# Performance work log

Hardware: AMD Instinct MI355X
Metric: run time of the kernel (lower is better)

The kernel has to match this reference:

```python
import jax, jax.numpy as jnp
import numpy as np

N_NODES = 100000
N_EDGES = 2000000
D_IN = 4
HID = 64


def setup_inputs() -> dict:
    key = jax.random.key(0)
    ks = jax.random.split(key, 8)
    node_feats = jax.random.normal(ks[0], (N_NODES, D_IN), dtype=jnp.float32)
    pairs = jax.random.randint(ks[1], (N_EDGES, 2), 0, N_NODES, dtype=jnp.int64)
    # Kaiming-ish init scaling
    W1 = jax.random.normal(ks[2], (D_IN, HID), dtype=jnp.float32) / np.sqrt(D_IN)
    b1 = jnp.zeros((HID,), dtype=jnp.float32)
    W2 = jax.random.normal(ks[3], (HID, HID), dtype=jnp.float32) / np.sqrt(HID)
    b2 = jnp.zeros((HID,), dtype=jnp.float32)
    We1 = jax.random.normal(ks[4], (3 * HID, HID), dtype=jnp.float32) / np.sqrt(3 * HID)
    be1 = jnp.zeros((HID,), dtype=jnp.float32)
    We2 = jax.random.normal(ks[5], (HID, 1), dtype=jnp.float32) / np.sqrt(HID)
    be2 = jnp.zeros((1,), dtype=jnp.float32)
    return {"node_feats": node_feats, "pairs": pairs, "W1": W1, "b1": b1,
            "W2": W2, "b2": b2, "We1": We1, "be1": be1, "We2": We2, "be2": be2}


def reference(node_feats, pairs, W1, b1, W2, b2, We1, be1, We2, be2):
    # node MLP: Linear -> ReLU -> Linear -> ReLU
    H = jax.nn.relu(node_feats @ W1 + b1)      # [N, HID]
    H = jax.nn.relu(H @ W2 + b2)               # [N, HID]
    # vectorized gather over all edge pairs (replaces Python loop)
    hu = H[pairs[:, 0]]                        # [E, HID]
    hv = H[pairs[:, 1]]                        # [E, HID]
    E = jnp.concatenate([hu, hv, jnp.abs(hu - hv)], axis=-1)  # [E, 3*HID]
    # edge MLP: Linear -> ReLU -> Linear, squeeze last dim
    scores = (jax.nn.relu(E @ We1 + be1) @ We2 + be2)[:, 0]   # [E]
    return scores
```

## Files before the change

### kernel.cpp

```cpp
#include <hip/hip_runtime.h>

#define N_NODES 100000
#define N_EDGES 2000000

typedef __bf16 bf16x8 __attribute__((ext_vector_type(8)));
typedef float f32x4 __attribute__((ext_vector_type(4)));
typedef float f32x16 __attribute__((ext_vector_type(16)));
typedef unsigned short u16x2 __attribute__((ext_vector_type(2)));

#define AS1 __attribute__((address_space(1)))
#define AS3 __attribute__((address_space(3)))

__device__ __forceinline__ unsigned f2bf_rne(float f) {
  unsigned u = __builtin_bit_cast(unsigned, f);
  u += 0x7FFFu + ((u >> 16) & 1u);
  return u >> 16;
}

__device__ __forceinline__ unsigned pack_rhu(float lo, float hi) {
  unsigned ulo = __builtin_bit_cast(unsigned, lo) + 0x8000u;
  unsigned uhi = __builtin_bit_cast(unsigned, hi) + 0x8000u;
  return __builtin_amdgcn_perm(uhi, ulo, 0x07060302u);
}

__device__ __forceinline__ unsigned pk_max_u16(unsigned a, unsigned b) {
  u16x2 r = __builtin_elementwise_max(__builtin_bit_cast(u16x2, a),
                                      __builtin_bit_cast(u16x2, b));
  return __builtin_bit_cast(unsigned, r);
}
__device__ __forceinline__ unsigned pk_min_u16(unsigned a, unsigned b) {
  u16x2 r = __builtin_elementwise_min(__builtin_bit_cast(u16x2, a),
                                      __builtin_bit_cast(u16x2, b));
  return __builtin_bit_cast(unsigned, r);
}

__global__ __launch_bounds__(64, 1) void node_mfma_kernel(
    const float* __restrict__ X, const float* __restrict__ W1,
    const float* __restrict__ b1, const float* __restrict__ W2,
    const float* __restrict__ b2, unsigned short* __restrict__ H) {
  const int lane = threadIdx.x;
  const int l15 = lane & 15;
  const int quad = lane >> 4;

  float w1v[2][4][8], b1v[2][8];
#pragma unroll
  for (int c = 0; c < 2; ++c)
#pragma unroll
    for (int j = 0; j < 8; ++j) {
      int col = c * 32 + quad * 8 + j;
      b1v[c][j] = b1[col];
#pragma unroll
      for (int d = 0; d < 4; ++d) w1v[c][d][j] = W1[d * 64 + col];
    }

  uint4 afr[2][4];
#pragma unroll
  for (int c = 0; c < 2; ++c)
#pragma unroll
    for (int mt = 0; mt < 4; ++mt) {
      unsigned w[4];
#pragma unroll
      for (int p = 0; p < 4; ++p) {
        int k = c * 32 + quad * 8 + 2 * p;
        unsigned lo = f2bf_rne(W2[k * 64 + mt * 16 + l15]);
        unsigned hi = f2bf_rne(W2[(k + 1) * 64 + mt * 16 + l15]);
        w[p] = lo | (hi << 16);
      }
      afr[c][mt] = make_uint4(w[0], w[1], w[2], w[3]);
    }
  float b2v[16];
#pragma unroll
  for (int mt = 0; mt < 4; ++mt)
#pragma unroll
    for (int r = 0; r < 4; ++r) b2v[mt * 4 + r] = b2[mt * 16 + quad * 4 + r];

  const int ntiles = N_NODES / 16;
  for (int tile = blockIdx.x; tile < ntiles; tile += gridDim.x) {
    float4 xv = ((const float4*)X)[tile * 16 + l15];

    uint4 bfr[2];
#pragma unroll
    for (int c = 0; c < 2; ++c) {
      unsigned w[4];
#pragma unroll
      for (int p = 0; p < 4; ++p) {
        float h0 = fmaxf(b1v[c][2 * p] + xv.x * w1v[c][0][2 * p] +
                             xv.y * w1v[c][1][2 * p] + xv.z * w1v[c][2][2 * p] +
                             xv.w * w1v[c][3][2 * p],
                         0.f);
        float h1 = fmaxf(b1v[c][2 * p + 1] + xv.x * w1v[c][0][2 * p + 1] +
                             xv.y * w1v[c][1][2 * p + 1] +
                             xv.z * w1v[c][2][2 * p + 1] +
                             xv.w * w1v[c][3][2 * p + 1],
                         0.f);
        w[p] = pack_rhu(h0, h1);
      }
      bfr[c] = make_uint4(w[0], w[1], w[2], w[3]);
    }

    f32x4 acc[4];
#pragma unroll
    for (int mt = 0; mt < 4; ++mt) acc[mt] = (f32x4){0.f, 0.f, 0.f, 0.f};
#pragma unroll
    for (int c = 0; c < 2; ++c)
#pragma unroll
      for (int mt = 0; mt < 4; ++mt)
        acc[mt] = __builtin_amdgcn_mfma_f32_16x16x32_bf16(
            __builtin_bit_cast(bf16x8, afr[c][mt]),
            __builtin_bit_cast(bf16x8, bfr[c]), acc[mt], 0, 0, 0);

    unsigned short* hrow = H + (tile * 16 + l15) * 64;
#pragma unroll
    for (int mt = 0; mt < 4; ++mt) {
      unsigned lo = pack_rhu(fmaxf(acc[mt][0] + b2v[mt * 4 + 0], 0.f),
                             fmaxf(acc[mt][1] + b2v[mt * 4 + 1], 0.f));
      unsigned hi = pack_rhu(fmaxf(acc[mt][2] + b2v[mt * 4 + 2], 0.f),
                             fmaxf(acc[mt][3] + b2v[mt * 4 + 3], 0.f));
      *(uint2*)(hrow + mt * 16 + quad * 4) = make_uint2(lo, hi);
    }
  }
}

__global__ __launch_bounds__(256, 2) void edge_mlp_kernel(
    const unsigned short* __restrict__ H, const int* __restrict__ pairs,
    const float* __restrict__ We1, const float* __restrict__ be1,
    const float* __restrict__ We2, const float* __restrict__ be2,
    float* __restrict__ out) {
  __shared__ uint4 gbuf[4][2][512];
  __shared__ uint4 scratch[64];
  __shared__ float lds_c[64];
  const int tid = threadIdx.x;
  const int lane = tid & 63;
  const int n = lane & 31;
  const int half = lane >> 5;
  const int wave = tid >> 6;
  const int rowsel = lane >> 3;
  const int swzc = (lane & 7) ^ rowsel;

  if (tid < 64) lds_c[tid] = We2[tid];

  uint4 afr[13][2];
#pragma unroll
  for (int c = 0; c < 12; ++c)
#pragma unroll
    for (int mt = 0; mt < 2; ++mt) {
      int col = mt * 32 + n;
      int kb = c * 16 + half * 8;
      unsigned w[4];
#pragma unroll
      for (int p = 0; p < 4; ++p)
        w[p] = f2bf_rne(We1[(kb + 2 * p) * 64 + col]) |
               (f2bf_rne(We1[(kb + 2 * p + 1) * 64 + col]) << 16);
      afr[c][mt] = make_uint4(w[0], w[1], w[2], w[3]);
    }
#pragma unroll
  for (int mt = 0; mt < 2; ++mt)
    afr[12][mt] =
        make_uint4((half == 0) ? f2bf_rne(be1[mt * 32 + n]) : 0u, 0u, 0u, 0u);

  const uint4 b13u = make_uint4((half == 0) ? 0x00003F80u : 0u, 0u, 0u, 0u);
  const float be2v = be2[0];

  uint4* const bufA = &gbuf[wave][0][0];
  uint4* const bufB = &gbuf[wave][1][0];
  int rbo[4];
#pragma unroll
  for (int c = 0; c < 4; ++c) rbo[c] = n * 8 + ((2 * c + half) ^ (n & 7));

  const int wid = blockIdx.x * 4 + wave;
  const int nw = gridDim.x * 4;
  const int ntiles = N_EDGES / 32;
  const int last = ntiles - 1;
  const int2* pairs2 = (const int2*)pairs;

  __syncthreads();

  auto issue_gathers = [&](uint4* dst, const int2* prs) {
#pragma unroll
    for (int k = 0; k < 4; ++k) {
      const AS1 unsigned* gu =
          (const AS1 unsigned*)(H + (size_t)prs[k].x * 64) + swzc * 4;
      const AS1 unsigned* gv =
          (const AS1 unsigned*)(H + (size_t)prs[k].y * 64) + swzc * 4;
      __builtin_amdgcn_global_load_lds(gu, (AS3 unsigned*)(dst + k * 64), 16,
                                       0, 0);
      __builtin_amdgcn_global_load_lds(
          gv, (AS3 unsigned*)(dst + 256 + k * 64), 16, 0, 0);
    }
  };

  int2 pr[4];
  {
#pragma unroll
    for (int k = 0; k < 4; ++k) pr[k] = pairs2[wid * 32 + k * 8 + rowsel];
    issue_gathers(bufA, pr);
    int t1 = wid + nw <= last ? wid + nw : last;
#pragma unroll
    for (int k = 0; k < 4; ++k) pr[k] = pairs2[t1 * 32 + k * 8 + rowsel];
    __builtin_amdgcn_global_load_lds((const AS1 unsigned*)H,
                                     (AS3 unsigned*)scratch, 16, 0, 0);
  }

  auto body = [&](int tc, uint4* CONS, uint4* FILL) {
    __builtin_amdgcn_sched_barrier(0);
    __builtin_amdgcn_s_waitcnt(0x0F75);
    __builtin_amdgcn_sched_barrier(0);

    issue_gathers(FILL, pr);
    __builtin_amdgcn_sched_barrier(0);
    {
      int tn = tc + 2 * nw <= last ? tc + 2 * nw : last;
#pragma unroll
      for (int k = 0; k < 4; ++k) pr[k] = pairs2[tn * 32 + k * 8 + rowsel];
    }

    const int t = tc <= last ? tc : last;
    uint4 hu[4], hv[4];
#pragma unroll
    for (int c = 0; c < 4; ++c) {
      hu[c] = CONS[rbo[c]];
      hv[c] = CONS[256 + rbo[c]];
    }
    uint4 pmx[4], pmn[4];
#pragma unroll
    for (int c = 0; c < 4; ++c) {
      pmx[c].x = pk_max_u16(hu[c].x, hv[c].x);
      pmx[c].y = pk_max_u16(hu[c].y, hv[c].y);
      pmx[c].z = pk_max_u16(hu[c].z, hv[c].z);
      pmx[c].w = pk_max_u16(hu[c].w, hv[c].w);
      pmn[c].x = pk_min_u16(hu[c].x, hv[c].x) | 0x80008000u;
      pmn[c].y = pk_min_u16(hu[c].y, hv[c].y) | 0x80008000u;
      pmn[c].z = pk_min_u16(hu[c].z, hv[c].z) | 0x80008000u;
      pmn[c].w = pk_min_u16(hu[c].w, hv[c].w) | 0x80008000u;
    }

    f32x16 acc[2];
    acc[0] = (f32x16)(0.f);
    acc[1] = (f32x16)(0.f);
#pragma unroll
    for (int c = 0; c < 4; ++c) {
      const bf16x8 b = __builtin_bit_cast(bf16x8, hu[c]);
#pragma unroll
      for (int mt = 0; mt < 2; ++mt)
        acc[mt] = __builtin_amdgcn_mfma_f32_32x32x16_bf16(
            __builtin_bit_cast(bf16x8, afr[c][mt]), b, acc[mt], 0, 0, 0);
    }
#pragma unroll
    for (int c = 0; c < 4; ++c) {
      const bf16x8 b = __builtin_bit_cast(bf16x8, hv[c]);
#pragma unroll
      for (int mt = 0; mt < 2; ++mt)
        acc[mt] = __builtin_amdgcn_mfma_f32_32x32x16_bf16(
            __builtin_bit_cast(bf16x8, afr[4 + c][mt]), b, acc[mt], 0, 0, 0);
    }
#pragma unroll
    for (int c = 0; c < 4; ++c) {
      const bf16x8 b = __builtin_bit_cast(bf16x8, pmx[c]);
#pragma unroll
      for (int mt = 0; mt < 2; ++mt)
        acc[mt] = __builtin_amdgcn_mfma_f32_32x32x16_bf16(
            __builtin_bit_cast(bf16x8, afr[8 + c][mt]), b, acc[mt], 0, 0, 0);
    }
#pragma unroll
    for (int c = 0; c < 4; ++c) {
      const bf16x8 b = __builtin_bit_cast(bf16x8, pmn[c]);
#pragma unroll
      for (int mt = 0; mt < 2; ++mt)
        acc[mt] = __builtin_amdgcn_mfma_f32_32x32x16_bf16(
            __builtin_bit_cast(bf16x8, afr[8 + c][mt]), b, acc[mt], 0, 0, 0);
    }
#pragma unroll
    for (int mt = 0; mt < 2; ++mt)
      acc[mt] = __builtin_amdgcn_mfma_f32_32x32x16_bf16(
          __builtin_bit_cast(bf16x8, afr[12][mt]),
          __builtin_bit_cast(bf16x8, b13u), acc[mt], 0, 0, 0);

    float s = 0.f;
#pragma unroll
    for (int mt = 0; mt < 2; ++mt)
#pragma unroll
      for (int g = 0; g < 4; ++g) {
        const float4 ew = *(const float4*)&lds_c[mt * 32 + g * 8 + 4 * half];
        s += fmaxf(acc[mt][4 * g + 0], 0.f) * ew.x;
        s += fmaxf(acc[mt][4 * g + 1], 0.f) * ew.y;
        s += fmaxf(acc[mt][4 * g + 2], 0.f) * ew.z;
        s += fmaxf(acc[mt][4 * g + 3], 0.f) * ew.w;
      }
    s += __shfl_xor(s, 32);
    if (half == 0) out[t * 32 + n] = s + be2v;
  };

  for (int t = wid; t < ntiles; t += 2 * nw) {
    body(t, bufA, bufB);
    body(t + nw, bufB, bufA);
  }
}

extern "C" void kernel_launch(void* const* d_in, const int* in_sizes, int n_in,
                              void* d_out, int out_size, void* d_ws,
                              size_t ws_size, hipStream_t stream) {
  const float* X = (const float*)d_in[0];
  const int* pairs = (const int*)d_in[1];
  const float* W1 = (const float*)d_in[2];
  const float* b1 = (const float*)d_in[3];
  const float* W2 = (const float*)d_in[4];
  const float* b2 = (const float*)d_in[5];
  const float* We1 = (const float*)d_in[6];
  const float* be1 = (const float*)d_in[7];
  const float* We2 = (const float*)d_in[8];
  const float* be2 = (const float*)d_in[9];
  float* out = (float*)d_out;
  unsigned short* H = (unsigned short*)d_ws;

  node_mfma_kernel<<<1024, 64, 0, stream>>>(X, W1, b1, W2, b2, H);
  edge_mlp_kernel<<<512, 256, 0, stream>>>(H, pairs, We1, be1, We2, be2, out);
}
```

Measured before the change: 166.9 us.

## Raise edge kernel occupancy by single-buffering gathers and moving weights to LDS

Switches the edge MLP from double-buffered LDS gathers to a single buffer per wave: the tile is read into registers, then the next gathers are issued into the same buffer. Half of the We1 fragments now live in LDS instead of registers. The |hu-hv| term is computed as a true float abs-diff (one MFMA chunk) rather than the max/min trick that needed two chunks. Together these cut MFMA work and register and LDS pressure so launch bounds and grid can go from 2 to 3 blocks per CU. The cost is less latency hiding per wave, extra LDS reads of weights on every tile, and more VALU work for the abs-diff conversion.

```diff
diff --git a/kernel.cpp b/kernel.cpp
--- a/kernel.cpp
+++ b/kernel.cpp
@@ -6,10 +6,12 @@
 typedef __bf16 bf16x8 __attribute__((ext_vector_type(8)));
 typedef float f32x4 __attribute__((ext_vector_type(4)));
 typedef float f32x16 __attribute__((ext_vector_type(16)));
-typedef unsigned short u16x2 __attribute__((ext_vector_type(2)));
 
 #define AS1 __attribute__((address_space(1)))
 #define AS3 __attribute__((address_space(3)))
+
+struct TrueTag { static constexpr bool value = true; };
+struct FalseTag { static constexpr bool value = false; };
 
 __device__ __forceinline__ unsigned f2bf_rne(float f) {
   unsigned u = __builtin_bit_cast(unsigned, f);
@@ -23,15 +25,12 @@
   return __builtin_amdgcn_perm(uhi, ulo, 0x07060302u);
 }
 
-__device__ __forceinline__ unsigned pk_max_u16(unsigned a, unsigned b) {
-  u16x2 r = __builtin_elementwise_max(__builtin_bit_cast(u16x2, a),
-                                      __builtin_bit_cast(u16x2, b));
-  return __builtin_bit_cast(unsigned, r);
-}
-__device__ __forceinline__ unsigned pk_min_u16(unsigned a, unsigned b) {
-  u16x2 r = __builtin_elementwise_min(__builtin_bit_cast(u16x2, a),
-                                      __builtin_bit_cast(u16x2, b));
-  return __builtin_bit_cast(unsigned, r);
+__device__ __forceinline__ unsigned absdiff_pack(unsigned a, unsigned b) {
+  float alo = __builtin_bit_cast(float, a << 16);
+  float ahi = __builtin_bit_cast(float, a & 0xFFFF0000u);
+  float blo = __builtin_bit_cast(float, b << 16);
+  float bhi = __builtin_bit_cast(float, b & 0xFFFF0000u);
+  return pack_rhu(fabsf(alo - blo), fabsf(ahi - bhi));
 }
 
 __global__ __launch_bounds__(64, 1) void node_mfma_kernel(
@@ -121,14 +120,15 @@
   }
 }
 
-__global__ __launch_bounds__(256, 2) void edge_mlp_kernel(
+__global__ __launch_bounds__(256, 3) void edge_mlp_kernel(
     const unsigned short* __restrict__ H, const int* __restrict__ pairs,
     const float* __restrict__ We1, const float* __restrict__ be1,
     const float* __restrict__ We2, const float* __restrict__ be2,
     float* __restrict__ out) {
-  __shared__ uint4 gbuf[4][2][512];
-  __shared__ uint4 scratch[64];
+  __shared__ uint4 gbuf[4][512];
+  __shared__ uint4 lds_w6[6][2][64];
   __shared__ float lds_c[64];
+
   const int tid = threadIdx.x;
   const int lane = tid & 63;
   const int n = lane & 31;
@@ -139,13 +139,28 @@
 
   if (tid < 64) lds_c[tid] = We2[tid];
 
-  uint4 afr[13][2];
-#pragma unroll
-  for (int c = 0; c < 12; ++c)
+#pragma unroll
+  for (int i = 0; i < 3; ++i) {
+    const int idx = wave * 3 + i;
+    const int c = 6 + (idx >> 1);
+    const int mt = idx & 1;
+    const int col = mt * 32 + n;
+    const int kb = c * 16 + half * 8;
+    unsigned w[4];
+#pragma unroll
+    for (int p = 0; p < 4; ++p)
+      w[p] = f2bf_rne(We1[(kb + 2 * p) * 64 + col]) |
+             (f2bf_rne(We1[(kb + 2 * p + 1) * 64 + col]) << 16);
+    lds_w6[c - 6][mt][lane] = make_uint4(w[0], w[1], w[2], w[3]);
+  }
+
+  uint4 afr[6][2];
+#pragma unroll
+  for (int c = 0; c < 6; ++c)
 #pragma unroll
     for (int mt = 0; mt < 2; ++mt) {
-      int col = mt * 32 + n;
-      int kb = c * 16 + half * 8;
+      const int col = mt * 32 + n;
+      const int kb = c * 16 + half * 8;
       unsigned w[4];
 #pragma unroll
       for (int p = 0; p < 4; ++p)
@@ -153,16 +168,14 @@
                (f2bf_rne(We1[(kb + 2 * p + 1) * 64 + col]) << 16);
       afr[c][mt] = make_uint4(w[0], w[1], w[2], w[3]);
     }
+  unsigned a12[2];
 #pragma unroll
   for (int mt = 0; mt < 2; ++mt)
-    afr[12][mt] =
-        make_uint4((half == 0) ? f2bf_rne(be1[mt * 32 + n]) : 0u, 0u, 0u, 0u);
-
+    a12[mt] = (half == 0) ? f2bf_rne(be1[mt * 32 + n]) : 0u;
   const uint4 b13u = make_uint4((half == 0) ? 0x00003F80u : 0u, 0u, 0u, 0u);
   const float be2v = be2[0];
 
-  uint4* const bufA = &gbuf[wave][0][0];
-  uint4* const bufB = &gbuf[wave][1][0];
+  uint4* const buf = &gbuf[wave][0];
   int rbo[4];
 #pragma unroll
   for (int c = 0; c < 4; ++c) rbo[c] = n * 8 + ((2 * c + half) ^ (n & 7));
@@ -193,20 +206,31 @@
   {
 #pragma unroll
     for (int k = 0; k < 4; ++k) pr[k] = pairs2[wid * 32 + k * 8 + rowsel];
-    issue_gathers(bufA, pr);
+    issue_gathers(buf, pr);
+    __builtin_amdgcn_sched_barrier(0);
     int t1 = wid + nw <= last ? wid + nw : last;
 #pragma unroll
     for (int k = 0; k < 4; ++k) pr[k] = pairs2[t1 * 32 + k * 8 + rowsel];
-    __builtin_amdgcn_global_load_lds((const AS1 unsigned*)H,
-                                     (AS3 unsigned*)scratch, 16, 0, 0);
   }
 
-  auto body = [&](int tc, uint4* CONS, uint4* FILL) {
-    __builtin_amdgcn_sched_barrier(0);
-    __builtin_amdgcn_s_waitcnt(0x0F75);
-    __builtin_amdgcn_sched_barrier(0);
-
-    issue_gathers(FILL, pr);
+  auto body = [&](int tc, auto FIRST) {
+    __builtin_amdgcn_sched_barrier(0);
+    if constexpr (decltype(FIRST)::value)
+      __builtin_amdgcn_s_waitcnt(0x0F74);
+    else
+      __builtin_amdgcn_s_waitcnt(0x0F75);
+    __builtin_amdgcn_sched_barrier(0);
+
+    const int t = tc <= last ? tc : last;
+    uint4 hu[4], hv[4];
+#pragma unroll
+    for (int c = 0; c < 4; ++c) {
+      hu[c] = buf[rbo[c]];
+      hv[c] = buf[256 + rbo[c]];
+    }
+    asm volatile("s_waitcnt lgkmcnt(0)" ::: "memory");
+    __builtin_amdgcn_sched_barrier(0);
+    issue_gathers(buf, pr);
     __builtin_amdgcn_sched_barrier(0);
     {
       int tn = tc + 2 * nw <= last ? tc + 2 * nw : last;
@@ -214,24 +238,13 @@
       for (int k = 0; k < 4; ++k) pr[k] = pairs2[tn * 32 + k * 8 + rowsel];
     }
 
-    const int t = tc <= last ? tc : last;
-    uint4 hu[4], hv[4];
+    uint4 ab[4];
 #pragma unroll
     for (int c = 0; c < 4; ++c) {
-      hu[c] = CONS[rbo[c]];
-      hv[c] = CONS[256 + rbo[c]];
-    }
-    uint4 pmx[4], pmn[4];
-#pragma unroll
-    for (int c = 0; c < 4; ++c) {
-      pmx[c].x = pk_max_u16(hu[c].x, hv[c].x);
-      pmx[c].y = pk_max_u16(hu[c].y, hv[c].y);
-      pmx[c].z = pk_max_u16(hu[c].z, hv[c].z);
-      pmx[c].w = pk_max_u16(hu[c].w, hv[c].w);
-      pmn[c].x = pk_min_u16(hu[c].x, hv[c].x) | 0x80008000u;
-      pmn[c].y = pk_min_u16(hu[c].y, hv[c].y) | 0x80008000u;
-      pmn[c].z = pk_min_u16(hu[c].z, hv[c].z) | 0x80008000u;
-      pmn[c].w = pk_min_u16(hu[c].w, hv[c].w) | 0x80008000u;
+      ab[c].x = absdiff_pack(hu[c].x, hv[c].x);
+      ab[c].y = absdiff_pack(hu[c].y, hv[c].y);
+      ab[c].z = absdiff_pack(hu[c].z, hv[c].z);
+      ab[c].w = absdiff_pack(hu[c].w, hv[c].w);
     }
 
     f32x16 acc[2];
@@ -246,7 +259,7 @@
             __builtin_bit_cast(bf16x8, afr[c][mt]), b, acc[mt], 0, 0, 0);
     }
 #pragma unroll
-    for (int c = 0; c < 4; ++c) {
+    for (int c = 0; c < 2; ++c) {
       const bf16x8 b = __builtin_bit_cast(bf16x8, hv[c]);
 #pragma unroll
       for (int mt = 0; mt < 2; ++mt)
@@ -254,25 +267,29 @@
             __builtin_bit_cast(bf16x8, afr[4 + c][mt]), b, acc[mt], 0, 0, 0);
     }
 #pragma unroll
+    for (int c = 0; c < 2; ++c) {
+      const bf16x8 b = __builtin_bit_cast(bf16x8, hv[2 + c]);
+#pragma unroll
+      for (int mt = 0; mt < 2; ++mt) {
+        const uint4 a = lds_w6[c][mt][lane];
+        acc[mt] = __builtin_amdgcn_mfma_f32_32x32x16_bf16(
+            __builtin_bit_cast(bf16x8, a), b, acc[mt], 0, 0, 0);
+      }
+    }
+#pragma unroll
     for (int c = 0; c < 4; ++c) {
-      const bf16x8 b = __builtin_bit_cast(bf16x8, pmx[c]);
-#pragma unroll
-      for (int mt = 0; mt < 2; ++mt)
+      const bf16x8 b = __builtin_bit_cast(bf16x8, ab[c]);
+#pragma unroll
+      for (int mt = 0; mt < 2; ++mt) {
+        const uint4 a = lds_w6[2 + c][mt][lane];
         acc[mt] = __builtin_amdgcn_mfma_f32_32x32x16_bf16(
-            __builtin_bit_cast(bf16x8, afr[8 + c][mt]), b, acc[mt], 0, 0, 0);
-    }
-#pragma unroll
-    for (int c = 0; c < 4; ++c) {
-      const bf16x8 b = __builtin_bit_cast(bf16x8, pmn[c]);
-#pragma unroll
-      for (int mt = 0; mt < 2; ++mt)
-        acc[mt] = __builtin_amdgcn_mfma_f32_32x32x16_bf16(
-            __builtin_bit_cast(bf16x8, afr[8 + c][mt]), b, acc[mt], 0, 0, 0);
+            __builtin_bit_cast(bf16x8, a), b, acc[mt], 0, 0, 0);
+      }
     }
 #pragma unroll
     for (int mt = 0; mt < 2; ++mt)
       acc[mt] = __builtin_amdgcn_mfma_f32_32x32x16_bf16(
-          __builtin_bit_cast(bf16x8, afr[12][mt]),
+          __builtin_bit_cast(bf16x8, make_uint4(a12[mt], 0u, 0u, 0u)),
           __builtin_bit_cast(bf16x8, b13u), acc[mt], 0, 0, 0);
 
     float s = 0.f;
@@ -290,10 +307,9 @@
     if (half == 0) out[t * 32 + n] = s + be2v;
   };
 
-  for (int t = wid; t < ntiles; t += 2 * nw) {
-    body(t, bufA, bufB);
-    body(t + nw, bufB, bufA);
-  }
+  int t = wid;
+  body(t, TrueTag{});
+  for (t += nw; t < ntiles; t += nw) body(t, FalseTag{});
 }
 
 extern "C" void kernel_launch(void* const* d_in, const int* in_sizes, int n_in,
@@ -313,5 +329,5 @@
   unsigned short* H = (unsigned short*)d_ws;
 
   node_mfma_kernel<<<1024, 64, 0, stream>>>(X, W1, b1, W2, b2, H);
-  edge_mlp_kernel<<<512, 256, 0, stream>>>(H, pairs, We1, be1, We2, be2, out);
-}
+  edge_mlp_kernel<<<768, 256, 0, stream>>>(H, pairs, We1, be1, We2, be2, out);
+}
```

Result: faster. 156.6 us (-6.2%).
